# Kernel optimization log

Measured on AMD Instinct MI355X. Metric: run time of the kernel, lower is better.

## Reference

```python
import jax, jax.numpy as jnp
import numpy as np

N = 100000   # nodes
F = 128      # input features
H = 128      # hidden = 2*output_dim
Z = 64       # output_dim
E = 1600000  # message-passing edges
EP = 200000  # pos/neg decode edges each


def setup_inputs() -> dict:
    key = jax.random.key(0)
    ks = jax.random.split(key, 6)
    x = jax.random.normal(ks[0], (N, F), dtype=jnp.float32)
    edge_index = jax.random.randint(ks[1], (2, E), 0, N, dtype=jnp.int64)
    pos_edge = jax.random.randint(ks[2], (2, EP), 0, N, dtype=jnp.int64)
    neg_edge = jax.random.randint(ks[3], (2, EP), 0, N, dtype=jnp.int64)
    W1 = jax.random.normal(ks[4], (F, H), dtype=jnp.float32) / np.float32(np.sqrt(F))
    b1 = jnp.zeros((H,), jnp.float32)
    W2 = jax.random.normal(ks[5], (H, Z), dtype=jnp.float32) / np.float32(np.sqrt(H))
    b2 = jnp.zeros((Z,), jnp.float32)
    return dict(x=x, W1=W1, b1=b1, W2=W2, b2=b2,
                edge_index=edge_index, pos_edge=pos_edge, neg_edge=neg_edge)


def _gcn_conv(x, src, dst, norm, W, b, n):
    # x' = scatter_add_dst(norm * (x @ W)[src]) + b   (GCNConv, sym-normalized, self-loops)
    h = x @ W                         # [N, out]
    msg = h[src] * norm[:, None]      # [E+N, out] gather + scale
    out = jax.ops.segment_sum(msg, dst, num_segments=n)
    return out + b


def reference(x, W1, b1, W2, b2, edge_index, pos_edge, neg_edge):
    # add self-loops (GCNConv default)
    loop = jnp.arange(N, dtype=edge_index.dtype)
    src = jnp.concatenate([edge_index[0], loop])
    dst = jnp.concatenate([edge_index[1], loop])
    # symmetric normalization deg^-1/2[src] * deg^-1/2[dst]
    deg = jax.ops.segment_sum(jnp.ones(dst.shape, x.dtype), dst, num_segments=N)
    dinv = jnp.where(deg > 0, jax.lax.rsqrt(deg), 0.0)
    norm = dinv[src] * dinv[dst]
    # encoder: GCN -> ReLU -> GCN
    h = jax.nn.relu(_gcn_conv(x, src, dst, norm, W1, b1, N))
    latent = _gcn_conv(h, src, dst, norm, W2, b2, N)
    # decoder: edge dot products on pos+neg edges
    e = jnp.concatenate([pos_edge, neg_edge], axis=-1)  # [2, 2*EP]
    logits = jnp.sum(latent[e[0]] * latent[e[1]], axis=-1)
    return logits
```

## Files before the change

kernel.cpp:

```cpp
#include <hip/hip_runtime.h>

#define N_NODES 100000
#define F_IN    128
#define H_DIM   128
#define Z_DIM   64
#define E_EDGES 1600000
#define EP_EDGES 200000

#define BSHIFT 7
#define NBUCK  ((N_NODES + 127) >> 7)
#define CHUNK  4096
#define NCHUNK ((E_EDGES + CHUNK - 1) / CHUNK)

typedef __attribute__((ext_vector_type(8))) short short8;
typedef __attribute__((ext_vector_type(4))) float f32x4;
typedef unsigned int uint;
typedef unsigned short ushort;

__device__ __forceinline__ ushort f2bf(float f) {
    uint u = __float_as_uint(f);
    u += 0x7fffu + ((u >> 16) & 1u);
    return (ushort)(u >> 16);
}
__device__ __forceinline__ float bflo(uint u) { return __uint_as_float(u << 16); }
__device__ __forceinline__ float bfhi(uint u) { return __uint_as_float(u & 0xffff0000u); }


__global__ __launch_bounds__(256) void wprep_kernel(const float* __restrict__ W1,
                                                    const float* __restrict__ W2,
                                                    ushort* __restrict__ W1T,
                                                    ushort* __restrict__ W2T,
                                                    int* __restrict__ gcur) {
    int i = blockIdx.x * 256 + threadIdx.x;
    if (i < 1024) gcur[i] = 0;
    if (i < 128 * 128) {
        int n = i >> 7, k = i & 127;
        W1T[i] = f2bf(W1[k * 128 + n]);
    }
    int j = i - 128 * 128;
    if (j >= 0 && j < 64 * 128) {
        int n = j >> 7, k = j & 127;
        W2T[j] = f2bf(W2[k * 64 + n]);
    }
}


__global__ __launch_bounds__(256) void bhist_kernel(const int* __restrict__ dst,
                                                    int* __restrict__ gcur,
                                                    int* __restrict__ tbl) {
    __shared__ int lh[NBUCK];
    for (int i = threadIdx.x; i < NBUCK; i += 256) lh[i] = 0;
    __syncthreads();
    int base = blockIdx.x * CHUNK;
    int end = min(base + CHUNK, E_EDGES);
    for (int e = base + threadIdx.x; e < end; e += 256)
        atomicAdd(&lh[dst[e] >> BSHIFT], 1);
    __syncthreads();
    int* trow = tbl + (size_t)blockIdx.x * NBUCK;
    for (int i = threadIdx.x; i < NBUCK; i += 256) {
        int c = lh[i];
        trow[i] = c;
        if (c) atomicAdd(&gcur[i], c);
    }
}


__global__ __launch_bounds__(1024) void bscan_kernel(int* __restrict__ gc) {
    __shared__ int s[1024];
    int t = threadIdx.x;
    int v = (t < NBUCK) ? gc[t] : 0;
    s[t] = v;
    __syncthreads();
    #pragma unroll
    for (int off = 1; off < 1024; off <<= 1) {
        int x = (t >= off) ? s[t - off] : 0;
        __syncthreads();
        s[t] += x;
        __syncthreads();
    }
    if (t < NBUCK) gc[t] = s[t] - v;
}


__global__ __launch_bounds__(512) void chunk_scan_kernel(int* __restrict__ tbl,
                                                         const int* __restrict__ gcur) {
    __shared__ int s[512];
    int b = blockIdx.x, t = threadIdx.x;
    int v = (t < NCHUNK) ? tbl[(size_t)t * NBUCK + b] : 0;
    s[t] = v;
    __syncthreads();
    #pragma unroll
    for (int off = 1; off < 512; off <<= 1) {
        int x = (t >= off) ? s[t - off] : 0;
        __syncthreads();
        s[t] += x;
        __syncthreads();
    }
    if (t < NCHUNK)
        tbl[(size_t)t * NBUCK + b] = gcur[b] + (s[t] - v);
}


__global__ __launch_bounds__(256) void bscatter_kernel(const int* __restrict__ src,
                                                       const int* __restrict__ dst,
                                                       const int* __restrict__ tbl,
                                                       int* __restrict__ sorted) {
    __shared__ int lbase[NBUCK];
    int c = blockIdx.x;
    const int* trow = tbl + (size_t)c * NBUCK;
    for (int i = threadIdx.x; i < NBUCK; i += 256) lbase[i] = trow[i];
    __syncthreads();
    int base = c * CHUNK;
    int end = min(base + CHUNK, E_EDGES);
    for (int e = base + threadIdx.x; e < end; e += 256) {
        int d = dst[e];
        int p = atomicAdd(&lbase[d >> BSHIFT], 1);
        sorted[p] = (src[e] << 7) | (d & 127);
    }
}


__global__ __launch_bounds__(256) void bucket_csr_kernel(const int* __restrict__ sorted,
                                                         const int* __restrict__ gcur,
                                                         int* __restrict__ csr,
                                                         int* __restrict__ ends,
                                                         float* __restrict__ dinv) {
    __shared__ int lcnt[4][128], lcur[4][128];
    int b = blockIdx.x, t = threadIdx.x;
    int wave = t >> 6;
    int bstart = gcur[b];
    int bend = (b + 1 < NBUCK) ? gcur[b + 1] : E_EDGES;
    if (t < 128) { lcnt[0][t] = 0; lcnt[1][t] = 0; }
    else { int u = t - 128; lcnt[2][u] = 0; lcnt[3][u] = 0; }
    __syncthreads();
    for (int i = bstart + t; i < bend; i += 256)
        atomicAdd(&lcnt[wave][sorted[i] & 127], 1);
    __syncthreads();
    if (t < 64) {
        int w0a = lcnt[0][t], w1a = lcnt[1][t], w2a = lcnt[2][t], w3a = lcnt[3][t];
        int w0b = lcnt[0][t + 64], w1b = lcnt[1][t + 64], w2b = lcnt[2][t + 64], w3b = lcnt[3][t + 64];
        int c0 = w0a + w1a + w2a + w3a;
        int c1 = w0b + w1b + w2b + w3b;
        int s0 = c0;
        #pragma unroll
        for (int d = 1; d < 64; d <<= 1) {
            int x = __shfl_up(s0, d, 64);
            if (t >= d) s0 += x;
        }
        int tot0 = __shfl(s0, 63, 64);
        int s1 = c1;
        #pragma unroll
        for (int d = 1; d < 64; d <<= 1) {
            int x = __shfl_up(s1, d, 64);
            if (t >= d) s1 += x;
        }
        s1 += tot0;
        int basea = bstart + s0 - c0;
        int baseb = bstart + s1 - c1;
        lcur[0][t] = basea;
        lcur[1][t] = basea + w0a;
        lcur[2][t] = basea + w0a + w1a;
        lcur[3][t] = basea + w0a + w1a + w2a;
        lcur[0][t + 64] = baseb;
        lcur[1][t + 64] = baseb + w0b;
        lcur[2][t + 64] = baseb + w0b + w1b;
        lcur[3][t + 64] = baseb + w0b + w1b + w2b;
        int n0 = b * 128 + t, n1 = n0 + 64;
        if (n0 < N_NODES) { ends[n0] = bstart + s0; dinv[n0] = rsqrtf(1.0f + (float)c0); }
        if (n1 < N_NODES) { ends[n1] = bstart + s1; dinv[n1] = rsqrtf(1.0f + (float)c1); }
    }
    __syncthreads();
    for (int i = bstart + t; i < bend; i += 256) {
        int v = sorted[i];
        int p = atomicAdd(&lcur[wave][v & 127], 1);
        csr[p] = v >> 7;
    }
}


template<int NC, bool A_F32>
__global__ __launch_bounds__(256) void gemm_mfma_kernel(const void* __restrict__ Ap,
                                                        const ushort* __restrict__ BT,
                                                        const float* __restrict__ dinv,
                                                        ushort* __restrict__ C, int M) {
    constexpr int NT = NC / 16;
    __shared__ ushort Bs[4 * NT * 64 * 8];

    for (int idx = threadIdx.x; idx < 4 * NT * 64; idx += 256) {
        int l   = idx & 63;
        int nt  = (idx >> 6) % NT;
        int kc  = idx / (64 * NT);
        int m16 = l & 15, quad = l >> 4;
        ((short8*)Bs)[idx] =
            *(const short8*)(BT + ((nt * 16 + m16) * 128 + kc * 32 + quad * 8));
    }
    __syncthreads();

    int wave = threadIdx.x >> 6, lane = threadIdx.x & 63;
    int m16 = lane & 15, quad = lane >> 4;
    int row0 = (blockIdx.x * 4 + wave) * 16;
    if (row0 >= M) return;
    int arow = row0 + m16;
    if (arow >= M) arow = M - 1;

    f32x4 acc[NT];
    #pragma unroll
    for (int t = 0; t < NT; ++t) acc[t] = (f32x4){0.f, 0.f, 0.f, 0.f};

    #pragma unroll
    for (int kc = 0; kc < 4; ++kc) {
        short8 a;
        if (A_F32) {
            const float* A = (const float*)Ap;
            const float4* p = (const float4*)(A + (size_t)arow * 128 + kc * 32 + quad * 8);
            float4 x0 = p[0], x1 = p[1];
            a[0] = (short)f2bf(x0.x); a[1] = (short)f2bf(x0.y);
            a[2] = (short)f2bf(x0.z); a[3] = (short)f2bf(x0.w);
            a[4] = (short)f2bf(x1.x); a[5] = (short)f2bf(x1.y);
            a[6] = (short)f2bf(x1.z); a[7] = (short)f2bf(x1.w);
        } else {
            a = *(const short8*)((const ushort*)Ap + (size_t)arow * 128 + kc * 32 + quad * 8);
        }
        #pragma unroll
        for (int nt = 0; nt < NT; ++nt) {
            short8 b = ((const short8*)Bs)[(kc * NT + nt) * 64 + lane];
            acc[nt] = __builtin_amdgcn_mfma_f32_16x16x32_bf16(a, b, acc[nt], 0, 0, 0);
        }
    }

    #pragma unroll
    for (int r = 0; r < 4; ++r) {
        int row = row0 + quad * 4 + r;
        if (row < M) {
            float dr = dinv[row];
            #pragma unroll
            for (int nt = 0; nt < NT; ++nt)
                C[(size_t)row * NC + nt * 16 + m16] = f2bf(acc[nt][r] * dr);
        }
    }
}


__global__ __launch_bounds__(256, 8) void gather128_kernel(const ushort* __restrict__ feat,
                                                           const float* __restrict__ bias,
                                                           const float* __restrict__ dinv,
                                                           const int* __restrict__ ends,
                                                           const int* __restrict__ csr,
                                                           ushort* __restrict__ out) {
    int wave = threadIdx.x >> 6, lane = threadIdx.x & 63;
    int n = blockIdx.x * 4 + wave;
    const uint* F = (const uint*)feat;
    uint rowoff = (uint)n * 64u + (uint)lane;

    uint su = F[rowoff];
    float l0 = bflo(su), h0 = bfhi(su);
    float l1 = 0.f, h1 = 0.f;

    int j0 = n ? ends[n - 1] : 0, j1 = ends[n];
    j0 = __builtin_amdgcn_readfirstlane(j0);
    j1 = __builtin_amdgcn_readfirstlane(j1);

    for (int base = j0; base < j1; base += 64) {
        int m = min(64, j1 - base);
        int idxv = csr[base + min(lane, m - 1)];
        int e = 0;
        for (; e + 8 <= m; e += 8) {
            int s0 = __builtin_amdgcn_readlane(idxv, e + 0);
            int s1 = __builtin_amdgcn_readlane(idxv, e + 1);
            int s2 = __builtin_amdgcn_readlane(idxv, e + 2);
            int s3 = __builtin_amdgcn_readlane(idxv, e + 3);
            int s4 = __builtin_amdgcn_readlane(idxv, e + 4);
            int s5 = __builtin_amdgcn_readlane(idxv, e + 5);
            int s6 = __builtin_amdgcn_readlane(idxv, e + 6);
            int s7 = __builtin_amdgcn_readlane(idxv, e + 7);
            uint r0 = F[(uint)s0 * 64u + (uint)lane];
            uint r1 = F[(uint)s1 * 64u + (uint)lane];
            uint r2 = F[(uint)s2 * 64u + (uint)lane];
            uint r3 = F[(uint)s3 * 64u + (uint)lane];
            uint r4 = F[(uint)s4 * 64u + (uint)lane];
            uint r5 = F[(uint)s5 * 64u + (uint)lane];
            uint r6 = F[(uint)s6 * 64u + (uint)lane];
            uint r7 = F[(uint)s7 * 64u + (uint)lane];
            l0 += bflo(r0) + bflo(r2);
            l1 += bflo(r1) + bflo(r3);
            h0 += bfhi(r0) + bfhi(r2);
            h1 += bfhi(r1) + bfhi(r3);
            l0 += bflo(r4) + bflo(r6);
            l1 += bflo(r5) + bflo(r7);
            h0 += bfhi(r4) + bfhi(r6);
            h1 += bfhi(r5) + bfhi(r7);
        }
        for (; e < m; ++e) {
            int s = __builtin_amdgcn_readlane(idxv, e);
            uint r = F[(uint)s * 64u + (uint)lane];
            l0 += bflo(r); h0 += bfhi(r);
        }
    }
    float dn = dinv[n];
    float2 bv = ((const float2*)bias)[lane];
    float rlo = fmaxf(bv.x + dn * (l0 + l1), 0.f);
    float rhi = fmaxf(bv.y + dn * (h0 + h1), 0.f);
    ((uint*)out)[rowoff] = (uint)f2bf(rlo) | ((uint)f2bf(rhi) << 16);
}


__global__ __launch_bounds__(256, 8) void gather64_kernel(const ushort* __restrict__ feat,
                                                          const float* __restrict__ bias,
                                                          const float* __restrict__ dinv,
                                                          const int* __restrict__ ends,
                                                          const int* __restrict__ csr,
                                                          ushort* __restrict__ outB) {
    int wave = threadIdx.x >> 6, lane = threadIdx.x & 63;
    int n = blockIdx.x * 4 + wave;
    uint rowoff = (uint)n * 64u + (uint)lane;

    float a0 = __uint_as_float((uint)feat[rowoff] << 16);
    float a1 = 0.f;

    int j0 = n ? ends[n - 1] : 0, j1 = ends[n];
    j0 = __builtin_amdgcn_readfirstlane(j0);
    j1 = __builtin_amdgcn_readfirstlane(j1);

    for (int base = j0; base < j1; base += 64) {
        int m = min(64, j1 - base);
        int idxv = csr[base + min(lane, m - 1)];
        int e = 0;
        for (; e + 8 <= m; e += 8) {
            int s0 = __builtin_amdgcn_readlane(idxv, e + 0);
            int s1 = __builtin_amdgcn_readlane(idxv, e + 1);
            int s2 = __builtin_amdgcn_readlane(idxv, e + 2);
            int s3 = __builtin_amdgcn_readlane(idxv, e + 3);
            int s4 = __builtin_amdgcn_readlane(idxv, e + 4);
            int s5 = __builtin_amdgcn_readlane(idxv, e + 5);
            int s6 = __builtin_amdgcn_readlane(idxv, e + 6);
            int s7 = __builtin_amdgcn_readlane(idxv, e + 7);
            uint r0 = feat[(uint)s0 * 64u + (uint)lane];
            uint r1 = feat[(uint)s1 * 64u + (uint)lane];
            uint r2 = feat[(uint)s2 * 64u + (uint)lane];
            uint r3 = feat[(uint)s3 * 64u + (uint)lane];
            uint r4 = feat[(uint)s4 * 64u + (uint)lane];
            uint r5 = feat[(uint)s5 * 64u + (uint)lane];
            uint r6 = feat[(uint)s6 * 64u + (uint)lane];
            uint r7 = feat[(uint)s7 * 64u + (uint)lane];
            a0 += __uint_as_float(r0 << 16) + __uint_as_float(r2 << 16);
            a1 += __uint_as_float(r1 << 16) + __uint_as_float(r3 << 16);
            a0 += __uint_as_float(r4 << 16) + __uint_as_float(r6 << 16);
            a1 += __uint_as_float(r5 << 16) + __uint_as_float(r7 << 16);
        }
        for (; e < m; ++e) {
            int s = __builtin_amdgcn_readlane(idxv, e);
            uint r = feat[(uint)s * 64u + (uint)lane];
            a0 += __uint_as_float(r << 16);
        }
    }
    float dn = dinv[n];
    float o = bias[lane] + dn * (a0 + a1);
    outB[rowoff] = f2bf(o);
}


__global__ __launch_bounds__(256) void decode_kernel(const ushort* __restrict__ latentB,
                                                     const int* __restrict__ pos,
                                                     const int* __restrict__ neg,
                                                     float* __restrict__ out) {
    int gwave = (blockIdx.x * 256 + threadIdx.x) >> 6;
    int lane = threadIdx.x & 63;
    int half = lane >> 5, sl = lane & 31;
    const uint* L = (const uint*)latentB;
    int e0 = gwave * 8 + half * 4;
    if (e0 >= 2 * EP_EDGES) return;

    int ia[4], ib[4];
    #pragma unroll
    for (int u = 0; u < 4; ++u) {
        int edge = e0 + u;
        if (edge < EP_EDGES) {
            ia[u] = pos[edge];
            ib[u] = pos[EP_EDGES + edge];
        } else {
            int e2 = edge - EP_EDGES;
            ia[u] = neg[e2];
            ib[u] = neg[EP_EDGES + e2];
        }
    }
    uint la[4], lb[4];
    #pragma unroll
    for (int u = 0; u < 4; ++u) {
        la[u] = L[(size_t)ia[u] * 32 + sl];
        lb[u] = L[(size_t)ib[u] * 32 + sl];
    }
    float v[4];
    #pragma unroll
    for (int u = 0; u < 4; ++u)
        v[u] = bflo(la[u]) * bflo(lb[u]) + bfhi(la[u]) * bfhi(lb[u]);
    #pragma unroll
    for (int u = 0; u < 4; ++u) {
        float s = v[u];
        #pragma unroll
        for (int off = 16; off > 0; off >>= 1) s += __shfl_down(s, off, 64);
        if (sl == 0) out[e0 + u] = s;
    }
}


extern "C" void kernel_launch(void* const* d_in, const int* in_sizes, int n_in,
                              void* d_out, int out_size, void* d_ws, size_t ws_size,
                              hipStream_t stream) {
    const float* x  = (const float*)d_in[0];
    const float* W1 = (const float*)d_in[1];
    const float* b1 = (const float*)d_in[2];
    const float* W2 = (const float*)d_in[3];
    const float* b2 = (const float*)d_in[4];
    const int* edge_index = (const int*)d_in[5];
    const int* pos = (const int*)d_in[6];
    const int* neg = (const int*)d_in[7];
    float* out = (float*)d_out;

    const int* src = edge_index;
    const int* dst = edge_index + E_EDGES;

    float*  dinv   = (float*)d_ws;
    int*    ends   = (int*)(dinv + N_NODES);
    int*    gcur   = ends + N_NODES;
    int*    tbl    = gcur + 1024;
    int*    sorted = tbl + NCHUNK * NBUCK;
    int*    csr    = sorted + E_EDGES;
    ushort* W1T    = (ushort*)(csr + E_EDGES);
    ushort* W2T    = W1T + 128 * 128;
    ushort* bufH   = (ushort*)(((uintptr_t)(W2T + 64 * 128) + 255) & ~(uintptr_t)255);
    ushort* bufR   = bufH + (size_t)N_NODES * 128;

    wprep_kernel<<<96, 256, 0, stream>>>(W1, W2, W1T, W2T, gcur);

    bhist_kernel<<<NCHUNK, 256, 0, stream>>>(dst, gcur, tbl);
    bscan_kernel<<<1, 1024, 0, stream>>>(gcur);
    chunk_scan_kernel<<<NBUCK, 512, 0, stream>>>(tbl, gcur);
    bscatter_kernel<<<NCHUNK, 256, 0, stream>>>(src, dst, tbl, sorted);
    bucket_csr_kernel<<<NBUCK, 256, 0, stream>>>(sorted, gcur, csr, ends, dinv);

    const int GEMM_GRID = (N_NODES + 63) / 64;

    gemm_mfma_kernel<128, true><<<GEMM_GRID, 256, 0, stream>>>(x, W1T, dinv, bufH, N_NODES);

    gather128_kernel<<<N_NODES / 4, 256, 0, stream>>>(bufH, b1, dinv, ends, csr, bufR);

    gemm_mfma_kernel<64, false><<<GEMM_GRID, 256, 0, stream>>>(bufR, W2T, dinv, bufH, N_NODES);

    ushort* latentB = bufR;
    gather64_kernel<<<N_NODES / 4, 256, 0, stream>>>(bufH, b2, dinv, ends, csr, latentB);

    decode_kernel<<<(2 * EP_EDGES) / 32, 256, 0, stream>>>(latentB, pos, neg, out);
}
```

Measured before the change: 320.0 us.

## Fuse layer-1 aggregation with second GEMM and pack 64-dim gather two edges per wave

The layer-1 neighbor aggregation now runs in a single-wave block that processes 16 rows, stages the ReLU output in shared memory, and multiplies it by W2 with MFMA. This removes the separate second GEMM launch and the round trip of the hidden activations through global memory. The 64-wide gather now has each half-wave load a different edge's row with 32-bit loads and combines the halves with a cross-lane shuffle. CSR index loads use nontemporal hints. The risk is lower parallelism: one wave handles 16 rows in sequence, so high-degree rows serialize latency and occupancy per block drops.

After: 312.4 us. 1.02x faster.

```diff
diff --git a/kernel.cpp b/kernel.cpp
--- a/kernel.cpp
+++ b/kernel.cpp
@@ -241,66 +241,90 @@
 }
 
 
-__global__ __launch_bounds__(256, 8) void gather128_kernel(const ushort* __restrict__ feat,
-                                                           const float* __restrict__ bias,
-                                                           const float* __restrict__ dinv,
-                                                           const int* __restrict__ ends,
-                                                           const int* __restrict__ csr,
-                                                           ushort* __restrict__ out) {
-    int wave = threadIdx.x >> 6, lane = threadIdx.x & 63;
-    int n = blockIdx.x * 4 + wave;
+__global__ __launch_bounds__(64, 4) void gather_gemm2_kernel(const ushort* __restrict__ feat,
+                                                             const float* __restrict__ bias,
+                                                             const float* __restrict__ dinv,
+                                                             const int* __restrict__ ends,
+                                                             const int* __restrict__ csr,
+                                                             const ushort* __restrict__ W2T,
+                                                             ushort* __restrict__ C) {
+    __shared__ uint T[16 * 68];
+    int lane = threadIdx.x;
+    int row0 = blockIdx.x * 16;
     const uint* F = (const uint*)feat;
-    uint rowoff = (uint)n * 64u + (uint)lane;
-
-    uint su = F[rowoff];
-    float l0 = bflo(su), h0 = bfhi(su);
-    float l1 = 0.f, h1 = 0.f;
-
-    int j0 = n ? ends[n - 1] : 0, j1 = ends[n];
-    j0 = __builtin_amdgcn_readfirstlane(j0);
-    j1 = __builtin_amdgcn_readfirstlane(j1);
-
-    for (int base = j0; base < j1; base += 64) {
-        int m = min(64, j1 - base);
-        int idxv = csr[base + min(lane, m - 1)];
-        int e = 0;
-        for (; e + 8 <= m; e += 8) {
-            int s0 = __builtin_amdgcn_readlane(idxv, e + 0);
-            int s1 = __builtin_amdgcn_readlane(idxv, e + 1);
-            int s2 = __builtin_amdgcn_readlane(idxv, e + 2);
-            int s3 = __builtin_amdgcn_readlane(idxv, e + 3);
-            int s4 = __builtin_amdgcn_readlane(idxv, e + 4);
-            int s5 = __builtin_amdgcn_readlane(idxv, e + 5);
-            int s6 = __builtin_amdgcn_readlane(idxv, e + 6);
-            int s7 = __builtin_amdgcn_readlane(idxv, e + 7);
-            uint r0 = F[(uint)s0 * 64u + (uint)lane];
-            uint r1 = F[(uint)s1 * 64u + (uint)lane];
-            uint r2 = F[(uint)s2 * 64u + (uint)lane];
-            uint r3 = F[(uint)s3 * 64u + (uint)lane];
-            uint r4 = F[(uint)s4 * 64u + (uint)lane];
-            uint r5 = F[(uint)s5 * 64u + (uint)lane];
-            uint r6 = F[(uint)s6 * 64u + (uint)lane];
-            uint r7 = F[(uint)s7 * 64u + (uint)lane];
-            l0 += bflo(r0) + bflo(r2);
-            l1 += bflo(r1) + bflo(r3);
-            h0 += bfhi(r0) + bfhi(r2);
-            h1 += bfhi(r1) + bfhi(r3);
-            l0 += bflo(r4) + bflo(r6);
-            l1 += bflo(r5) + bflo(r7);
-            h0 += bfhi(r4) + bfhi(r6);
-            h1 += bfhi(r5) + bfhi(r7);
-        }
-        for (; e < m; ++e) {
-            int s = __builtin_amdgcn_readlane(idxv, e);
-            uint r = F[(uint)s * 64u + (uint)lane];
-            l0 += bflo(r); h0 += bfhi(r);
-        }
-    }
-    float dn = dinv[n];
     float2 bv = ((const float2*)bias)[lane];
-    float rlo = fmaxf(bv.x + dn * (l0 + l1), 0.f);
-    float rhi = fmaxf(bv.y + dn * (h0 + h1), 0.f);
-    ((uint*)out)[rowoff] = (uint)f2bf(rlo) | ((uint)f2bf(rhi) << 16);
+
+    for (int i = 0; i < 16; ++i) {
+        int n = row0 + i;
+        uint su = F[(uint)n * 64u + (uint)lane];
+        float l0 = bflo(su), h0 = bfhi(su);
+        float l1 = 0.f, h1 = 0.f;
+        int j0 = n ? ends[n - 1] : 0, j1 = ends[n];
+        j0 = __builtin_amdgcn_readfirstlane(j0);
+        j1 = __builtin_amdgcn_readfirstlane(j1);
+        for (int base = j0; base < j1; base += 64) {
+            int m = min(64, j1 - base);
+            int idxv = __builtin_nontemporal_load(csr + base + min(lane, m - 1));
+            int e = 0;
+            for (; e + 8 <= m; e += 8) {
+                int s0 = __builtin_amdgcn_readlane(idxv, e + 0);
+                int s1 = __builtin_amdgcn_readlane(idxv, e + 1);
+                int s2 = __builtin_amdgcn_readlane(idxv, e + 2);
+                int s3 = __builtin_amdgcn_readlane(idxv, e + 3);
+                int s4 = __builtin_amdgcn_readlane(idxv, e + 4);
+                int s5 = __builtin_amdgcn_readlane(idxv, e + 5);
+                int s6 = __builtin_amdgcn_readlane(idxv, e + 6);
+                int s7 = __builtin_amdgcn_readlane(idxv, e + 7);
+                uint r0 = F[(uint)s0 * 64u + (uint)lane];
+                uint r1 = F[(uint)s1 * 64u + (uint)lane];
+                uint r2 = F[(uint)s2 * 64u + (uint)lane];
+                uint r3 = F[(uint)s3 * 64u + (uint)lane];
+                uint r4 = F[(uint)s4 * 64u + (uint)lane];
+                uint r5 = F[(uint)s5 * 64u + (uint)lane];
+                uint r6 = F[(uint)s6 * 64u + (uint)lane];
+                uint r7 = F[(uint)s7 * 64u + (uint)lane];
+                l0 += bflo(r0) + bflo(r2);
+                l1 += bflo(r1) + bflo(r3);
+                h0 += bfhi(r0) + bfhi(r2);
+                h1 += bfhi(r1) + bfhi(r3);
+                l0 += bflo(r4) + bflo(r6);
+                l1 += bflo(r5) + bflo(r7);
+                h0 += bfhi(r4) + bfhi(r6);
+                h1 += bfhi(r5) + bfhi(r7);
+            }
+            for (; e < m; ++e) {
+                int s = __builtin_amdgcn_readlane(idxv, e);
+                uint r = F[(uint)s * 64u + (uint)lane];
+                l0 += bflo(r); h0 += bfhi(r);
+            }
+        }
+        float dn = dinv[n];
+        float rlo = fmaxf(bv.x + dn * (l0 + l1), 0.f);
+        float rhi = fmaxf(bv.y + dn * (h0 + h1), 0.f);
+        T[i * 68 + lane] = (uint)f2bf(rlo) | ((uint)f2bf(rhi) << 16);
+    }
+
+    int m16 = lane & 15, quad = lane >> 4;
+    f32x4 acc[4];
+    #pragma unroll
+    for (int t = 0; t < 4; ++t) acc[t] = (f32x4){0.f, 0.f, 0.f, 0.f};
+    #pragma unroll
+    for (int kc = 0; kc < 4; ++kc) {
+        short8 a = *(const short8*)&T[m16 * 68 + kc * 16 + quad * 4];
+        #pragma unroll
+        for (int nt = 0; nt < 4; ++nt) {
+            short8 b = *(const short8*)(W2T + ((nt * 16 + m16) * 128 + kc * 32 + quad * 8));
+            acc[nt] = __builtin_amdgcn_mfma_f32_16x16x32_bf16(a, b, acc[nt], 0, 0, 0);
+        }
+    }
+    #pragma unroll
+    for (int r = 0; r < 4; ++r) {
+        int row = row0 + quad * 4 + r;
+        float dr = dinv[row];
+        #pragma unroll
+        for (int nt = 0; nt < 4; ++nt)
+            C[(size_t)row * 64 + nt * 16 + m16] = f2bf(acc[nt][r] * dr);
+    }
 }
 
 
@@ -311,11 +335,13 @@
                                                           const int* __restrict__ csr,
                                                           ushort* __restrict__ outB) {
     int wave = threadIdx.x >> 6, lane = threadIdx.x & 63;
+    int g = lane >> 5, c = lane & 31;
     int n = blockIdx.x * 4 + wave;
-    uint rowoff = (uint)n * 64u + (uint)lane;
-
-    float a0 = __uint_as_float((uint)feat[rowoff] << 16);
-    float a1 = 0.f;
+    const uint* F = (const uint*)feat;
+
+    float a0 = 0.f, a1 = 0.f;
+    uint su = F[(uint)n * 32u + (uint)c];
+    if (g == 0) { a0 = bflo(su); a1 = bfhi(su); }
 
     int j0 = n ? ends[n - 1] : 0, j1 = ends[n];
     j0 = __builtin_amdgcn_readfirstlane(j0);
@@ -323,39 +349,52 @@
 
     for (int base = j0; base < j1; base += 64) {
         int m = min(64, j1 - base);
-        int idxv = csr[base + min(lane, m - 1)];
+        int idxv = __builtin_nontemporal_load(csr + base + min(lane, m - 1));
         int e = 0;
         for (; e + 8 <= m; e += 8) {
-            int s0 = __builtin_amdgcn_readlane(idxv, e + 0);
-            int s1 = __builtin_amdgcn_readlane(idxv, e + 1);
-            int s2 = __builtin_amdgcn_readlane(idxv, e + 2);
-            int s3 = __builtin_amdgcn_readlane(idxv, e + 3);
-            int s4 = __builtin_amdgcn_readlane(idxv, e + 4);
-            int s5 = __builtin_amdgcn_readlane(idxv, e + 5);
-            int s6 = __builtin_amdgcn_readlane(idxv, e + 6);
-            int s7 = __builtin_amdgcn_readlane(idxv, e + 7);
-            uint r0 = feat[(uint)s0 * 64u + (uint)lane];
-            uint r1 = feat[(uint)s1 * 64u + (uint)lane];
-            uint r2 = feat[(uint)s2 * 64u + (uint)lane];
-            uint r3 = feat[(uint)s3 * 64u + (uint)lane];
-            uint r4 = feat[(uint)s4 * 64u + (uint)lane];
-            uint r5 = feat[(uint)s5 * 64u + (uint)lane];
-            uint r6 = feat[(uint)s6 * 64u + (uint)lane];
-            uint r7 = feat[(uint)s7 * 64u + (uint)lane];
-            a0 += __uint_as_float(r0 << 16) + __uint_as_float(r2 << 16);
-            a1 += __uint_as_float(r1 << 16) + __uint_as_float(r3 << 16);
-            a0 += __uint_as_float(r4 << 16) + __uint_as_float(r6 << 16);
-            a1 += __uint_as_float(r5 << 16) + __uint_as_float(r7 << 16);
-        }
-        for (; e < m; ++e) {
+            int sa0 = __builtin_amdgcn_readlane(idxv, e + 0);
+            int sb0 = __builtin_amdgcn_readlane(idxv, e + 1);
+            int sa1 = __builtin_amdgcn_readlane(idxv, e + 2);
+            int sb1 = __builtin_amdgcn_readlane(idxv, e + 3);
+            int sa2 = __builtin_amdgcn_readlane(idxv, e + 4);
+            int sb2 = __builtin_amdgcn_readlane(idxv, e + 5);
+            int sa3 = __builtin_amdgcn_readlane(idxv, e + 6);
+            int sb3 = __builtin_amdgcn_readlane(idxv, e + 7);
+            uint p0 = (uint)(g ? sb0 : sa0);
+            uint p1 = (uint)(g ? sb1 : sa1);
+            uint p2 = (uint)(g ? sb2 : sa2);
+            uint p3 = (uint)(g ? sb3 : sa3);
+            uint r0 = F[p0 * 32u + (uint)c];
+            uint r1 = F[p1 * 32u + (uint)c];
+            uint r2 = F[p2 * 32u + (uint)c];
+            uint r3 = F[p3 * 32u + (uint)c];
+            a0 += bflo(r0) + bflo(r1);
+            a1 += bfhi(r0) + bfhi(r1);
+            a0 += bflo(r2) + bflo(r3);
+            a1 += bfhi(r2) + bfhi(r3);
+        }
+        for (; e + 2 <= m; e += 2) {
+            int sa = __builtin_amdgcn_readlane(idxv, e);
+            int sb = __builtin_amdgcn_readlane(idxv, e + 1);
+            uint p = (uint)(g ? sb : sa);
+            uint r = F[p * 32u + (uint)c];
+            a0 += bflo(r); a1 += bfhi(r);
+        }
+        if (e < m) {
             int s = __builtin_amdgcn_readlane(idxv, e);
-            uint r = feat[(uint)s * 64u + (uint)lane];
-            a0 += __uint_as_float(r << 16);
-        }
-    }
-    float dn = dinv[n];
-    float o = bias[lane] + dn * (a0 + a1);
-    outB[rowoff] = f2bf(o);
+            uint r = F[(uint)s * 32u + (uint)c];
+            if (g == 0) { a0 += bflo(r); a1 += bfhi(r); }
+        }
+    }
+    a0 += __shfl_xor(a0, 32, 64);
+    a1 += __shfl_xor(a1, 32, 64);
+    if (g == 0) {
+        float dn = dinv[n];
+        float2 bv = ((const float2*)bias)[c];
+        float o0 = bv.x + dn * a0;
+        float o1 = bv.y + dn * a1;
+        ((uint*)outB)[(uint)n * 32u + (uint)c] = (uint)f2bf(o0) | ((uint)f2bf(o1) << 16);
+    }
 }
 
 
@@ -442,12 +481,10 @@
 
     gemm_mfma_kernel<128, true><<<GEMM_GRID, 256, 0, stream>>>(x, W1T, dinv, bufH, N_NODES);
 
-    gather128_kernel<<<N_NODES / 4, 256, 0, stream>>>(bufH, b1, dinv, ends, csr, bufR);
-
-    gemm_mfma_kernel<64, false><<<GEMM_GRID, 256, 0, stream>>>(bufR, W2T, dinv, bufH, N_NODES);
-
-    ushort* latentB = bufR;
-    gather64_kernel<<<N_NODES / 4, 256, 0, stream>>>(bufH, b2, dinv, ends, csr, latentB);
+    gather_gemm2_kernel<<<N_NODES / 16, 64, 0, stream>>>(bufH, b1, dinv, ends, csr, W2T, bufR);
+
+    ushort* latentB = bufH;
+    gather64_kernel<<<N_NODES / 4, 256, 0, stream>>>(bufR, b2, dinv, ends, csr, latentB);
 
     decode_kernel<<<(2 * EP_EDGES) / 32, 256, 0, stream>>>(latentB, pos, neg, out);
 }
```
